# Performance work log

Hardware: AMD Instinct MI355X
Metric: run time of the kernel (lower is better)

The kernel has to match this reference:

```python
import jax, jax.numpy as jnp
import numpy as np

NUM_HEADS = 4
NUM_GROUPS = 8
EPS = 1e-5


def setup_inputs() -> dict:
    key = jax.random.key(0)
    ks = jax.random.split(key, 4)
    b, c, h, w = 16, 512, 32, 32
    x = jax.random.normal(ks[0], (b, c, h, w), dtype=jnp.float32)
    norm_gamma = jnp.ones((c,), dtype=jnp.float32)
    norm_beta = jnp.zeros((c,), dtype=jnp.float32)
    qkv_w = jax.random.normal(ks[1], (3 * c, c), dtype=jnp.float32) * (c ** -0.5)
    qkv_b = jnp.zeros((3 * c,), dtype=jnp.float32)
    proj_w = jax.random.normal(ks[2], (c, c), dtype=jnp.float32) * (c ** -0.5)
    proj_b = jnp.zeros((c,), dtype=jnp.float32)
    return {"x": x, "norm_gamma": norm_gamma, "norm_beta": norm_beta,
            "qkv_w": qkv_w, "qkv_b": qkv_b, "proj_w": proj_w, "proj_b": proj_b}


def reference(x, norm_gamma, norm_beta, qkv_w, qkv_b, proj_w, proj_b):
    b, c, h, w = x.shape
    nh = NUM_HEADS
    dh = c // nh
    n = h * w
    # GroupNorm(8, c): normalize over (c/G, h, w) within each group, biased var
    xg = x.reshape(b, NUM_GROUPS, -1)
    mu = jnp.mean(xg, axis=-1, keepdims=True)
    var = jnp.var(xg, axis=-1, keepdims=True)
    xn = ((xg - mu) * jax.lax.rsqrt(var + EPS)).reshape(b, c, h, w)
    xn = xn * norm_gamma[:, None, None] + norm_beta[:, None, None]
    # QKV 1x1 conv == channel matmul
    qkv = jnp.einsum('oc,bchw->bohw', qkv_w, xn) + qkv_b[:, None, None]
    q, k, v = jnp.split(qkv, 3, axis=1)  # each [b, c, h, w]

    def to_heads(t):  # [b, c, h, w] -> [b, nh, n, dh]
        return t.reshape(b, nh, dh, n).transpose(0, 1, 3, 2)

    q, k, v = to_heads(q), to_heads(k), to_heads(v)
    scale = dh ** -0.5
    attn = jax.nn.softmax(jnp.einsum('bhnd,bhmd->bhnm', q, k) * scale, axis=-1)
    out = jnp.einsum('bhnm,bhmd->bhnd', attn, v)  # [b, nh, n, dh]
    out = out.transpose(0, 1, 3, 2).reshape(b, c, h, w)
    out = jnp.einsum('oc,bchw->bohw', proj_w, out) + proj_b[:, None, None]
    return x + out
```

## Files before the change

### kernel.cpp

```cpp
#include <hip/hip_runtime.h>

typedef unsigned short u16;
typedef unsigned int   u32;

typedef __attribute__((ext_vector_type(8)))  short bf16x8;
typedef __attribute__((ext_vector_type(16))) float f32x16;
typedef __attribute__((ext_vector_type(2)))  unsigned int u32x2;
#define MFMA32(a, b, c) __builtin_amdgcn_mfma_f32_32x32x16_bf16(a, b, c, 0, 0, 0)

__device__ __forceinline__ float bf2f(u16 h) { return __uint_as_float(((u32)h) << 16); }
__device__ __forceinline__ u16 f2bf(float f) {
  u32 u = __float_as_uint(f);
  u += 0x7fffu + ((u >> 16) & 1u);
  return (u16)(u >> 16);
}
__device__ __forceinline__ void unpack8(uint4 u, float* f) {
  f[0] = __uint_as_float(u.x << 16); f[1] = __uint_as_float(u.x & 0xffff0000u);
  f[2] = __uint_as_float(u.y << 16); f[3] = __uint_as_float(u.y & 0xffff0000u);
  f[4] = __uint_as_float(u.z << 16); f[5] = __uint_as_float(u.z & 0xffff0000u);
  f[6] = __uint_as_float(u.w << 16); f[7] = __uint_as_float(u.w & 0xffff0000u);
}
__device__ __forceinline__ void unpack4(uint2 u, float* f) {
  f[0] = __uint_as_float(u.x << 16); f[1] = __uint_as_float(u.x & 0xffff0000u);
  f[2] = __uint_as_float(u.y << 16); f[3] = __uint_as_float(u.y & 0xffff0000u);
}

template <bool F>
__device__ __forceinline__ void load8(const void* p, size_t idx, float* f) {
  if constexpr (F) {
    const float4* q = (const float4*)((const float*)p + idx);
    float4 a = q[0], b = q[1];
    f[0] = a.x; f[1] = a.y; f[2] = a.z; f[3] = a.w;
    f[4] = b.x; f[5] = b.y; f[6] = b.z; f[7] = b.w;
  } else {
    unpack8(*(const uint4*)((const u16*)p + idx), f);
  }
}
template <bool F>
__device__ __forceinline__ void load4(const void* p, size_t idx, float* f) {
  if constexpr (F) {
    float4 a = *(const float4*)((const float*)p + idx);
    f[0] = a.x; f[1] = a.y; f[2] = a.z; f[3] = a.w;
  } else {
    unpack4(*(const uint2*)((const u16*)p + idx), f);
  }
}
template <bool F>
__device__ __forceinline__ float load1(const void* p, size_t idx) {
  if constexpr (F) return ((const float*)p)[idx];
  else return bf2f(((const u16*)p)[idx]);
}

__device__ __forceinline__ void gl2lds16(const void* g, void* l) {
  __builtin_amdgcn_global_load_lds(
      (const __attribute__((address_space(1))) void*)g,
      (__attribute__((address_space(3))) void*)l, 16, 0, 0);
}

__global__ void detect_dtype(const void* __restrict__ x, int* __restrict__ flag) {
  if (threadIdx.x == 0 && blockIdx.x == 0) {
    const u32* p = (const u32*)x;
    int sane = 0;
    for (int i = 0; i < 256; ++i) {
      u32 e = (p[i] >> 7) & 0xFFu;
      sane += (e >= 100u && e <= 150u) ? 1 : 0;
    }
    *flag = (sane < 192) ? 1 : 0;
  }
}

__global__ void signal_ws(u16* __restrict__ out, int n) {
  int i = blockIdx.x * 256 + threadIdx.x;
  if (i < n) out[i] = 0x42C8;
}

#define SM_SCALE 0.08838834764831843f
#define QSC 0.12751743f


__global__ void __launch_bounds__(256) wconv_rt(const void* __restrict__ qkvw,
                                                const void* __restrict__ qkvb,
                                                u16* __restrict__ dst,
                                                const int* __restrict__ flag) {
  const bool F = (flag[0] != 0);
  int i = (blockIdx.x * 256 + threadIdx.x) * 8;
  if (i >= 787968) return;
  if (!F) {
    uint4 v = (i < 786432) ? *(const uint4*)((const u16*)qkvw + i)
                           : *(const uint4*)((const u16*)qkvb + (i - 786432));
    *(uint4*)(dst + i) = v;
  } else {
    const float* src = (i < 786432) ? ((const float*)qkvw + i)
                                    : ((const float*)qkvb + (i - 786432));
    float f[8];
    float4 a = *(const float4*)src, b = *(const float4*)(src + 4);
    f[0]=a.x; f[1]=a.y; f[2]=a.z; f[3]=a.w; f[4]=b.x; f[5]=b.y; f[6]=b.z; f[7]=b.w;
    u32 w0 = (u32)f2bf(f[0]) | ((u32)f2bf(f[1]) << 16);
    u32 w1 = (u32)f2bf(f[2]) | ((u32)f2bf(f[3]) << 16);
    u32 w2 = (u32)f2bf(f[4]) | ((u32)f2bf(f[5]) << 16);
    u32 w3 = (u32)f2bf(f[6]) | ((u32)f2bf(f[7]) << 16);
    *(uint4*)(dst + i) = make_uint4(w0, w1, w2, w3);
  }
}

template <bool F>
__device__ __forceinline__ void gn_norm_body(
    const void* __restrict__ x, const void* __restrict__ gamma,
    const void* __restrict__ beta, u16* __restrict__ xT,
    int g, int b, int tid,
    float* ssum, float* ssq, float* scb, float* bsb, float (*Tf)[64][65]) {
  const size_t base = (size_t)(b * 512 + g * 64) * 1024;
  float sum = 0.f, sq = 0.f;
  for (int i = tid; i < 8192; i += 256) {
    float f[8]; load8<F>(x, base + (size_t)i * 8, f);
#pragma unroll
    for (int m = 0; m < 8; ++m) { sum += f[m]; sq += f[m] * f[m]; }
  }
  ssum[tid] = sum; ssq[tid] = sq; __syncthreads();
  for (int off = 128; off > 0; off >>= 1) {
    if (tid < off) { ssum[tid] += ssum[tid + off]; ssq[tid] += ssq[tid + off]; }
    __syncthreads();
  }
  if (tid < 64) {
    float mu  = ssum[0] * (1.f / 65536.f);
    float var = ssq[0] * (1.f / 65536.f) - mu * mu;
    float s = load1<F>(gamma, g * 64 + tid) * rsqrtf(var + 1e-5f);
    scb[tid] = s;
    bsb[tid] = load1<F>(beta, g * 64 + tid) - mu * s;
  }
  __syncthreads();

  for (int s0 = 0; s0 < 1024; s0 += 64) {
    const int pb = (s0 >> 6) & 1;
#pragma unroll
    for (int half = 0; half < 2; ++half) {
      int idx = tid + half * 256;
      int c_loc = idx >> 3, s8 = (idx & 7) * 8;
      float f[8];
      load8<F>(x, base + (size_t)c_loc * 1024 + s0 + s8, f);
      float sm = scb[c_loc], ba = bsb[c_loc];
#pragma unroll
      for (int m = 0; m < 8; ++m) Tf[pb][s8 + m][c_loc] = f[m] * sm + ba;
    }
    __syncthreads();
#pragma unroll
    for (int half = 0; half < 2; ++half) {
      int idx = tid + half * 256;
      int s_loc = idx >> 3, c8 = (idx & 7) * 8;
      u32 pk[4];
#pragma unroll
      for (int m = 0; m < 4; ++m)
        pk[m] = (u32)f2bf(Tf[pb][s_loc][c8 + 2 * m]) |
                ((u32)f2bf(Tf[pb][s_loc][c8 + 2 * m + 1]) << 16);
      *(uint4*)(xT + (size_t)(b * 1024 + s0 + s_loc) * 512 + g * 64 + c8) =
          make_uint4(pk[0], pk[1], pk[2], pk[3]);
    }
  }
}

__global__ void __launch_bounds__(256) gn_norm_rt(const void* __restrict__ x,
                                                  const void* __restrict__ gamma,
                                                  const void* __restrict__ beta,
                                                  u16* __restrict__ xT,
                                                  const int* __restrict__ flag) {
  __shared__ float ssum[256], ssq[256], scb[64], bsb[64];
  __shared__ float Tf[2][64][65];
  const int g = blockIdx.x, b = blockIdx.y, tid = threadIdx.x;
  if (flag[0] != 0) gn_norm_body<true >(x, gamma, beta, xT, g, b, tid, ssum, ssq, scb, bsb, Tf);
  else              gn_norm_body<false>(x, gamma, beta, xT, g, b, tid, ssum, ssq, scb, bsb, Tf);
}

__global__ void __launch_bounds__(256, 4)
gemm_qkv(const u16* __restrict__ xT, const u16* __restrict__ wbf,
         u16* __restrict__ qkT, u16* __restrict__ Vbuf) {
  const bool vrole = (blockIdx.y >= 8);
  const int n0 = blockIdx.x * 128;
  const int m0 = (vrole ? (int)blockIdx.y - 8 : (int)blockIdx.y) * 128;
  const int b  = blockIdx.z;
  __shared__ __align__(16) u16 At[8192];
  __shared__ __align__(16) u16 Bt[8192];
  const int tid = threadIdx.x;
  const int w = tid >> 6, lane = tid & 63;
  const int lo = lane & 31, hi = lane >> 5;
  const int wm = w >> 1, wn = w & 1;
  const u16* bias = wbf + 786432;
  const u16* Ab = vrole ? (wbf + 524288) : (xT + (size_t)b * 524288);
  const u16* Bb = vrole ? (xT + (size_t)b * 524288) : wbf;
  u16* outp = vrole ? (Vbuf + (size_t)b * 524288) : (qkT + (size_t)b * 1048576);
  const int srow = lane >> 3, spc = lane & 7;

  f32x16 cA[2][2];
#pragma unroll
  for (int i = 0; i < 2; ++i)
#pragma unroll
    for (int j = 0; j < 2; ++j)
#pragma unroll
      for (int r = 0; r < 16; ++r) cA[i][j][r] = 0.f;

  for (int kt = 0; kt < 8; ++kt) {
    const int kb = kt * 64;
#pragma unroll
    for (int c = 0; c < 4; ++c) {
      int grp = w * 4 + c;
      int row = grp * 8 + srow;
      int lc  = spc ^ (row & 7);
      gl2lds16(Ab + (size_t)(m0 + row) * 512 + kb + lc * 8, &At[grp * 512]);
      gl2lds16(Bb + (size_t)(n0 + row) * 512 + kb + lc * 8, &Bt[grp * 512]);
    }
    __syncthreads();
#pragma unroll
    for (int k16 = 0; k16 < 4; ++k16) {
      const int lc = k16 * 2 + hi;
      const int rA0 = wm * 64 + lo,  rA1 = rA0 + 32;
      const int rB0 = wn * 64 + lo,  rB1 = rB0 + 32;
      bf16x8 a0 = *(const bf16x8*)&At[rA0 * 64 + ((lc ^ (rA0 & 7)) << 3)];
      bf16x8 a1 = *(const bf16x8*)&At[rA1 * 64 + ((lc ^ (rA1 & 7)) << 3)];
      bf16x8 b0 = *(const bf16x8*)&Bt[rB0 * 64 + ((lc ^ (rB0 & 7)) << 3)];
      bf16x8 b1 = *(const bf16x8*)&Bt[rB1 * 64 + ((lc ^ (rB1 & 7)) << 3)];
      cA[0][0] = MFMA32(a0, b0, cA[0][0]);
      cA[0][1] = MFMA32(a0, b1, cA[0][1]);
      cA[1][0] = MFMA32(a1, b0, cA[1][0]);
      cA[1][1] = MFMA32(a1, b1, cA[1][1]);
    }
    __syncthreads();
  }

  float bcol[2] = {0.f, 0.f};
  if (!vrole) {
    bcol[0] = bf2f(bias[n0 + wn * 64 + lo]);
    bcol[1] = bf2f(bias[n0 + wn * 64 + 32 + lo]);
  }
#pragma unroll
  for (int mt = 0; mt < 2; ++mt)
#pragma unroll
    for (int nt = 0; nt < 2; ++nt) {
      const int nbase = n0 + wn * 64 + nt * 32;
#pragma unroll
      for (int r = 0; r < 16; ++r) {
        int m = m0 + wm * 64 + mt * 32 + (r & 3) + 8 * (r >> 2) + 4 * hi;
        int n = nbase + lo;
        float v = cA[mt][nt][r];
        if (!vrole) {
          v += bcol[nt];
          if (nbase < 512) v *= QSC;
        } else {
          v += bf2f(bias[1024 + m]);
        }
        outp[(size_t)m * 1024 + n] = f2bf(v);
      }
    }
}

template <bool F>
__device__ __forceinline__ void proj_body(const void* __restrict__ A,
                                          const u16* __restrict__ B,
                                          const void* __restrict__ bias,
                                          const void* __restrict__ resid,
                                          void* __restrict__ outp,
                                          int n0, int m0, int b, int tid,
                                          u16 (*At)[72], u16 (*Bt)[72]) {
  const int w = tid >> 6, lane = tid & 63;
  const int lo = lane & 31, hi = lane >> 5;
  const int wm = w >> 1, wn = w & 1;
  const size_t bBase = (size_t)b * 524288;

  f32x16 cA[2][2];
#pragma unroll
  for (int i = 0; i < 2; ++i)
#pragma unroll
    for (int j = 0; j < 2; ++j)
#pragma unroll
      for (int r = 0; r < 16; ++r) cA[i][j][r] = 0.f;

  for (int kt = 0; kt < 8; ++kt) {
#pragma unroll
    for (int i = 0; i < 4; ++i) {
      int idx = tid + i * 256;
      int row = idx >> 3, kc = (idx & 7) * 8;
      int k = kt * 64 + kc;
      {
        if constexpr (F) {
          float f[8]; load8<true>(A, (size_t)(m0 + row) * 512 + k, f);
          u32 w0 = (u32)f2bf(f[0]) | ((u32)f2bf(f[1]) << 16);
          u32 w1 = (u32)f2bf(f[2]) | ((u32)f2bf(f[3]) << 16);
          u32 w2 = (u32)f2bf(f[4]) | ((u32)f2bf(f[5]) << 16);
          u32 w3 = (u32)f2bf(f[6]) | ((u32)f2bf(f[7]) << 16);
          *(uint4*)&At[row][kc] = make_uint4(w0, w1, w2, w3);
        } else {
          *(uint4*)&At[row][kc] =
              *(const uint4*)((const u16*)A + (size_t)(m0 + row) * 512 + k);
        }
      }
      *(uint4*)&Bt[row][kc] =
          *(const uint4*)(B + bBase + (size_t)(n0 + row) * 512 + k);
    }
    __syncthreads();
#pragma unroll
    for (int k16 = 0; k16 < 4; ++k16) {
      const int ko = k16 * 16 + hi * 8;
      bf16x8 a0 = *(const bf16x8*)&At[wm * 64 + lo][ko];
      bf16x8 a1 = *(const bf16x8*)&At[wm * 64 + 32 + lo][ko];
      bf16x8 b0 = *(const bf16x8*)&Bt[wn * 64 + lo][ko];
      bf16x8 b1 = *(const bf16x8*)&Bt[wn * 64 + 32 + lo][ko];
      cA[0][0] = MFMA32(a0, b0, cA[0][0]);
      cA[0][1] = MFMA32(a0, b1, cA[0][1]);
      cA[1][0] = MFMA32(a1, b0, cA[1][0]);
      cA[1][1] = MFMA32(a1, b1, cA[1][1]);
    }
    __syncthreads();
  }

#pragma unroll
  for (int mt = 0; mt < 2; ++mt)
#pragma unroll
    for (int nt = 0; nt < 2; ++nt) {
#pragma unroll
      for (int r = 0; r < 16; ++r) {
        int m = m0 + wm * 64 + mt * 32 + (r & 3) + 8 * (r >> 2) + 4 * hi;
        int n = n0 + wn * 64 + nt * 32 + lo;
        float v = cA[mt][nt][r];
        v += load1<F>(bias, m);
        v += load1<F>(resid, bBase + (size_t)m * 1024 + n);
        size_t off = bBase + (size_t)m * 1024 + n;
        if constexpr (F) ((float*)outp)[off] = v;
        else             ((u16*)outp)[off] = f2bf(v);
      }
    }
}

__global__ void __launch_bounds__(256, 4)
proj_rt(const void* __restrict__ projw, const u16* __restrict__ aout,
        const void* __restrict__ projb, const void* __restrict__ x,
        void* __restrict__ outp, const int* __restrict__ flag) {
  __shared__ __align__(16) u16 At[128][72];
  __shared__ __align__(16) u16 Bt[128][72];
  const int n0 = blockIdx.x * 128, m0 = blockIdx.y * 128, b = blockIdx.z;
  if (flag[0] != 0) proj_body<true >(projw, aout, projb, x, outp, n0, m0, b, threadIdx.x, At, Bt);
  else              proj_body<false>(projw, aout, projb, x, outp, n0, m0, b, threadIdx.x, At, Bt);
}

__global__ void __launch_bounds__(256, 2) attn4(const u16* __restrict__ qkT,
                                                const u16* __restrict__ V,
                                                u16* __restrict__ aout) {
  const int bh = blockIdx.x;
  const int q0 = blockIdx.y * 128;
  const int b = bh >> 2, h = bh & 3;
  const u16* qt = qkT + (size_t)b * 1048576;
  const u16* vb = V + (size_t)b * 524288 + (size_t)(h * 128) * 1024;
  __shared__ __align__(16) u16 smem[32768];
  const int tid = threadIdx.x;
  const int w = tid >> 6, lane = tid & 63;
  const int lo = lane & 31, hi = lane >> 5;

#pragma unroll
  for (int c = 0; c < 8; ++c) {
    int grp = w * 8 + c;
    int row = grp * 4 + (lane >> 4);
    int lc  = (lane & 15) ^ (row & 7);
    gl2lds16(qt + (size_t)(q0 + row) * 1024 + h * 128 + lc * 8, &smem[grp * 512]);
  }
#pragma unroll
  for (int c = 0; c < 4; ++c) {
    int grp = w * 4 + c;
    { int row = grp * 4 + (lane >> 4);
      int lc  = (lane & 15) ^ (row & 7);
      gl2lds16(qt + (size_t)row * 1024 + 512 + h * 128 + lc * 8,
               &smem[16384 + grp * 512]); }
    { int row = grp * 8 + (lane >> 3);
      int lc  = (lane & 7) ^ (row & 7);
      gl2lds16(vb + (size_t)row * 1024 + lc * 8,
               &smem[16384 + 8192 + grp * 512]); }
  }
  __syncthreads();
  bf16x8 qf[8];
  {
    const int row = 32 * w + lo;
#pragma unroll
    for (int k16 = 0; k16 < 8; ++k16) {
      int lc = k16 * 2 + hi;
      qf[k16] = *(const bf16x8*)&smem[row * 128 + ((lc ^ (row & 7)) << 3)];
    }
  }
  __syncthreads();

  f32x16 o[4];
  float lp = 0.f;
#pragma unroll
  for (int dt = 0; dt < 4; ++dt)
#pragma unroll
    for (int r = 0; r < 16; ++r) o[dt][r] = 0.f;

  for (int kt = 0; kt < 16; ++kt) {
    const u16* rb = &smem[((kt & 1) ^ 1) << 14];
    u16* wbuf = &smem[(kt & 1) << 14];

    if (kt < 15) {
      const int k0n = (kt + 1) * 64;
#pragma unroll
      for (int c = 0; c < 4; ++c) {
        int grp = w * 4 + c;
        { int row = grp * 4 + (lane >> 4);
          int lc  = (lane & 15) ^ (row & 7);
          gl2lds16(qt + (size_t)(k0n + row) * 1024 + 512 + h * 128 + lc * 8,
                   wbuf + grp * 512); }
        { int row = grp * 8 + (lane >> 3);
          int lc  = (lane & 7) ^ (row & 7);
          gl2lds16(vb + (size_t)row * 1024 + k0n + lc * 8,
                   wbuf + 8192 + grp * 512); }
      }
    }

    f32x16 s0, s1;
#pragma unroll
    for (int r = 0; r < 16; ++r) { s0[r] = 0.f; s1[r] = 0.f; }
#pragma unroll
    for (int k16 = 0; k16 < 8; ++k16) {
      const int lc = k16 * 2 + hi;
      const int r0 = lo, r1 = lo + 32;
      bf16x8 kf0 = *(const bf16x8*)&rb[r0 * 128 + ((lc ^ (r0 & 7)) << 3)];
      bf16x8 kf1 = *(const bf16x8*)&rb[r1 * 128 + ((lc ^ (r1 & 7)) << 3)];
      s0 = MFMA32(kf0, qf[k16], s0);
      s1 = MFMA32(kf1, qf[k16], s1);
    }

#pragma unroll
    for (int r = 0; r < 16; ++r) {
      s0[r] = exp2f(s0[r]);
      s1[r] = exp2f(s1[r]);
      lp += s0[r] + s1[r];
    }

    bf16x8 pa[4];
#define MKPA(ps, rb0, dst) do {                                               \
      u32 qa0, qa1, qb0, qb1;                                                 \
      asm("v_cvt_pk_bf16_f32 %0, %1, %2" : "=v"(qa0)                          \
          : "v"((ps)[(rb0) + 0]), "v"((ps)[(rb0) + 1]));                      \
      asm("v_cvt_pk_bf16_f32 %0, %1, %2" : "=v"(qa1)                          \
          : "v"((ps)[(rb0) + 2]), "v"((ps)[(rb0) + 3]));                      \
      asm("v_cvt_pk_bf16_f32 %0, %1, %2" : "=v"(qb0)                          \
          : "v"((ps)[(rb0) + 4]), "v"((ps)[(rb0) + 5]));                      \
      asm("v_cvt_pk_bf16_f32 %0, %1, %2" : "=v"(qb1)                          \
          : "v"((ps)[(rb0) + 6]), "v"((ps)[(rb0) + 7]));                      \
      u32x2 r0 = __builtin_amdgcn_permlane32_swap(qa0, qb0, false, false);    \
      u32x2 r1 = __builtin_amdgcn_permlane32_swap(qa1, qb1, false, false);    \
      union { u32 u[4]; bf16x8 v8; } pk_;                                     \
      pk_.u[0] = r0[0]; pk_.u[1] = r1[0]; pk_.u[2] = r0[1]; pk_.u[3] = r1[1]; \
      dst = pk_.v8;                                                           \
    } while (0)
    MKPA(s0, 0, pa[0]);
    MKPA(s0, 8, pa[1]);
    MKPA(s1, 0, pa[2]);
    MKPA(s1, 8, pa[3]);
#undef MKPA

#pragma unroll
    for (int t = 0; t < 4; ++t) {
      const int lc = t * 2 + hi;
#pragma unroll
      for (int dt = 0; dt < 4; ++dt) {
        const int row = dt * 32 + lo;
        bf16x8 bv = *(const bf16x8*)&rb[8192 + row * 64 + ((lc ^ (row & 7)) << 3)];
        o[dt] = MFMA32(pa[t], bv, o[dt]);
      }
    }
    __syncthreads();
  }

  float linv = 1.f / (lp + __shfl_xor(lp, 32));
#pragma unroll
  for (int r = 0; r < 16; ++r) {
    int pat = (r & 3) + 8 * (r >> 2) + 4 * hi;
    float lr = __shfl(linv, pat);
    int q = q0 + 32 * w + pat;
    size_t base = (size_t)(b * 1024 + q) * 512 + h * 128;
    aout[base +  0 + lo] = f2bf(o[0][r] * lr);
    aout[base + 32 + lo] = f2bf(o[1][r] * lr);
    aout[base + 64 + lo] = f2bf(o[2][r] * lr);
    aout[base + 96 + lo] = f2bf(o[3][r] * lr);
  }
}


template <bool F>
__global__ void __launch_bounds__(256) gn_stats(const void* __restrict__ x,
                                                const void* __restrict__ gamma,
                                                const void* __restrict__ beta,
                                                float* __restrict__ sc,
                                                float* __restrict__ bs,
                                                const int* __restrict__ flag) {
  if ((flag[0] != 0) != F) return;
  const int g = blockIdx.x, b = blockIdx.y;
  const int tid = threadIdx.x;
  const size_t base = (size_t)(b * 512 + g * 64) * 1024;
  float sum = 0.f, sq = 0.f;
  for (int i = tid; i < 8192; i += 256) {
    float f[8]; load8<F>(x, base + (size_t)i * 8, f);
#pragma unroll
    for (int m = 0; m < 8; ++m) { sum += f[m]; sq += f[m] * f[m]; }
  }
  __shared__ float ssum[256], ssq[256];
  ssum[tid] = sum; ssq[tid] = sq; __syncthreads();
  for (int off = 128; off > 0; off >>= 1) {
    if (tid < off) { ssum[tid] += ssum[tid + off]; ssq[tid] += ssq[tid + off]; }
    __syncthreads();
  }
  if (tid < 64) {
    float mu  = ssum[0] * (1.f / 65536.f);
    float var = ssq[0] * (1.f / 65536.f) - mu * mu;
    int c = g * 64 + tid;
    float s = load1<F>(gamma, c) * rsqrtf(var + 1e-5f);
    sc[b * 512 + c] = s;
    bs[b * 512 + c] = load1<F>(beta, c) - mu * s;
  }
}

template <bool F, bool BEXT, bool FOUT>
__global__ void __launch_bounds__(256) gemm64(const void* __restrict__ A,
                                              const void* __restrict__ B,
                                              const float* __restrict__ sc,
                                              const float* __restrict__ bs,
                                              const void* __restrict__ bias,
                                              const void* __restrict__ resid,
                                              void* __restrict__ outp,
                                              int mrows, int donorm, int bstride,
                                              const int* __restrict__ flag) {
  if ((flag[0] != 0) != F) return;
  const int s0 = blockIdx.x * 64;
  const int o0 = blockIdx.y * 64;
  const int b  = blockIdx.z;
  __shared__ __align__(16) float At[64][36];
  __shared__ __align__(16) float Bt[64][36];
  const int tid = threadIdx.x;
  const int ty = tid >> 4, tx = tid & 15;
  const int i0 = ty * 4, j0 = tx * 4;
  const int arow = tid >> 2, akc = (tid & 3) * 8;
  const int brow = tid >> 3, bnc = (tid & 7) * 8;
  float acc[4][4] = {};

  for (int kt = 0; kt < 512; kt += 32) {
    float af[8];
    load8<F>(A, (size_t)(o0 + arow) * 512 + akc + kt, af);
    *(float4*)&At[arow][akc]     = make_float4(af[0], af[1], af[2], af[3]);
    *(float4*)&At[arow][akc + 4] = make_float4(af[4], af[5], af[6], af[7]);
    const int c = kt + brow;
    float bf[8];
    load8<(BEXT && F)>(B, (size_t)(b * bstride + c) * 1024 + s0 + bnc, bf);
    float smul = 1.f, badd = 0.f;
    if (donorm) { smul = sc[b * 512 + c]; badd = bs[b * 512 + c]; }
#pragma unroll
    for (int m = 0; m < 8; ++m) Bt[bnc + m][brow] = bf[m] * smul + badd;
    __syncthreads();
#pragma unroll
    for (int kq = 0; kq < 8; ++kq) {
      float4 a0 = *(const float4*)&At[i0 + 0][kq * 4];
      float4 a1 = *(const float4*)&At[i0 + 1][kq * 4];
      float4 a2 = *(const float4*)&At[i0 + 2][kq * 4];
      float4 a3 = *(const float4*)&At[i0 + 3][kq * 4];
      float4 c0 = *(const float4*)&Bt[j0 + 0][kq * 4];
      float4 c1 = *(const float4*)&Bt[j0 + 1][kq * 4];
      float4 c2 = *(const float4*)&Bt[j0 + 2][kq * 4];
      float4 c3 = *(const float4*)&Bt[j0 + 3][kq * 4];
#define DOT4(ii, jj, AV, CV) acc[ii][jj] += AV.x * CV.x + AV.y * CV.y + AV.z * CV.z + AV.w * CV.w;
      DOT4(0,0,a0,c0) DOT4(0,1,a0,c1) DOT4(0,2,a0,c2) DOT4(0,3,a0,c3)
      DOT4(1,0,a1,c0) DOT4(1,1,a1,c1) DOT4(1,2,a1,c2) DOT4(1,3,a1,c3)
      DOT4(2,0,a2,c0) DOT4(2,1,a2,c1) DOT4(2,2,a2,c2) DOT4(2,3,a2,c3)
      DOT4(3,0,a3,c0) DOT4(3,1,a3,c1) DOT4(3,2,a3,c2) DOT4(3,3,a3,c3)
#undef DOT4
    }
    __syncthreads();
  }
#pragma unroll
  for (int ii = 0; ii < 4; ++ii) {
    const int o = o0 + i0 + ii;
    const float bb = load1<F>(bias, o);
    float v[4];
#pragma unroll
    for (int jj = 0; jj < 4; ++jj) v[jj] = acc[ii][jj] + bb;
    if (resid) {
      float xf[4];
      load4<F>(resid, (size_t)(b * 512 + o) * 1024 + s0 + j0, xf);
#pragma unroll
      for (int jj = 0; jj < 4; ++jj) v[jj] += xf[jj];
    }
    const size_t ooff = (size_t)(b * mrows + o) * 1024 + s0 + j0;
    if constexpr (FOUT) {
      *(float4*)((float*)outp + ooff) = make_float4(v[0], v[1], v[2], v[3]);
    } else {
      uint2 pk;
      pk.x = (u32)f2bf(v[0]) | ((u32)f2bf(v[1]) << 16);
      pk.y = (u32)f2bf(v[2]) | ((u32)f2bf(v[3]) << 16);
      *(uint2*)((u16*)outp + ooff) = pk;
    }
  }
}

__global__ void __launch_bounds__(256, 2) attn_old(u16* __restrict__ qkv) {
  const int q0 = blockIdx.x * 128;
  const int bh = blockIdx.y;
  const int b = bh >> 2, h = bh & 3;
  u16* qp = qkv + (size_t)(b * 1536 + h * 128) * 1024;
  const u16* kp = qp + (size_t)512 * 1024;
  const u16* vp = qp + (size_t)1024 * 1024;
  __shared__ __align__(16) u16 Qt[128][136];
  __shared__ __align__(16) u16 Kt[32][136];
  __shared__ __align__(16) u16 Vt[128][40];
  __shared__ __align__(16) u16 Pt[128][40];
  const int tid = threadIdx.x;
  const int w = tid >> 6, lane = tid & 63;
  const int lo = lane & 31, hi = lane >> 5;

  for (int idx = tid; idx < 2048; idx += 256) {
    int d = idx >> 4, s8 = (idx & 15) * 8;
    uint4 qv = *(const uint4*)(qp + (size_t)d * 1024 + q0 + s8);
    const u16* qs = (const u16*)&qv;
#pragma unroll
    for (int m = 0; m < 8; ++m) Qt[s8 + m][d] = qs[m];
  }
  __syncthreads();
  bf16x8 qf[8];
#pragma unroll
  for (int kq = 0; kq < 8; ++kq)
    qf[kq] = *(const bf16x8*)&Qt[32 * w + lo][kq * 16 + hi * 8];

  f32x16 o0, o1, o2, o3;
  float lp[16];
#pragma unroll
  for (int r = 0; r < 16; ++r) { o0[r] = 0.f; o1[r] = 0.f; o2[r] = 0.f; o3[r] = 0.f; lp[r] = 0.f; }

  for (int kt = 0; kt < 32; ++kt) {
    const int k0 = kt * 32;
    __syncthreads();
    for (int idx = tid; idx < 512; idx += 256) {
      int d = idx >> 2, s8 = (idx & 3) * 8;
      uint4 kv = *(const uint4*)(kp + (size_t)d * 1024 + k0 + s8);
      const u16* ks = (const u16*)&kv;
#pragma unroll
      for (int m = 0; m < 8; ++m) Kt[s8 + m][d] = ks[m];
      *(uint4*)&Vt[d][s8] = *(const uint4*)(vp + (size_t)d * 1024 + k0 + s8);
    }
    __syncthreads();
    f32x16 acc;
#pragma unroll
    for (int r = 0; r < 16; ++r) acc[r] = 0.f;
#pragma unroll
    for (int kq = 0; kq < 8; ++kq) {
      bf16x8 bq = *(const bf16x8*)&Kt[lo][kq * 16 + hi * 8];
      acc = MFMA32(qf[kq], bq, acc);
    }
#pragma unroll
    for (int r = 0; r < 16; ++r) {
      float pe = __expf(acc[r] * SM_SCALE);
      lp[r] += pe;
      int row = (r & 3) + 8 * (r >> 2) + 4 * hi;
      Pt[32 * w + row][lo] = f2bf(pe);
    }
    __syncthreads();
#pragma unroll
    for (int kq2 = 0; kq2 < 2; ++kq2) {
      bf16x8 a2 = *(const bf16x8*)&Pt[32 * w + lo][kq2 * 16 + hi * 8];
      bf16x8 b0 = *(const bf16x8*)&Vt[ 0 + lo][kq2 * 16 + hi * 8];
      bf16x8 b1 = *(const bf16x8*)&Vt[32 + lo][kq2 * 16 + hi * 8];
      bf16x8 b2 = *(const bf16x8*)&Vt[64 + lo][kq2 * 16 + hi * 8];
      bf16x8 b3 = *(const bf16x8*)&Vt[96 + lo][kq2 * 16 + hi * 8];
      o0 = MFMA32(a2, b0, o0);
      o1 = MFMA32(a2, b1, o1);
      o2 = MFMA32(a2, b2, o2);
      o3 = MFMA32(a2, b3, o3);
    }
  }
#pragma unroll
  for (int r = 0; r < 16; ++r) {
    float su = lp[r];
    su += __shfl_xor(su, 1);  su += __shfl_xor(su, 2);
    su += __shfl_xor(su, 4);  su += __shfl_xor(su, 8);
    su += __shfl_xor(su, 16);
    float linv = 1.f / su;
    int row = (r & 3) + 8 * (r >> 2) + 4 * hi;
    int q = q0 + 32 * w + row;
    size_t base = (size_t)(b * 1536 + h * 128) * 1024 + q;
    qkv[base + (size_t)( 0 + lo) * 1024] = f2bf(o0[r] * linv);
    qkv[base + (size_t)(32 + lo) * 1024] = f2bf(o1[r] * linv);
    qkv[base + (size_t)(64 + lo) * 1024] = f2bf(o2[r] * linv);
    qkv[base + (size_t)(96 + lo) * 1024] = f2bf(o3[r] * linv);
  }
}

extern "C" void kernel_launch(void* const* d_in, const int* in_sizes, int n_in,
                              void* d_out, int out_size, void* d_ws, size_t ws_size,
                              hipStream_t stream) {
  const void* x     = d_in[0];
  const void* gamma = d_in[1];
  const void* beta  = d_in[2];
  const void* qkvw  = d_in[3];
  const void* qkvb  = d_in[4];
  const void* projw = d_in[5];
  const void* projb = d_in[6];

  char* ws = (char*)d_ws;
  const size_t MB = 1024 * 1024;
  const size_t FAST_NEED = 64 * MB + 64;
  const size_t OLD_NEED  = 48 * MB + 256 + 2 * 16 * 512 * 4;

  if (ws_size >= FAST_NEED) {
    u16* xT   = (u16*)ws;
    u16* qkT  = (u16*)(ws + 16 * MB);
    u16* Vbuf = (u16*)(ws + 48 * MB);
    int* flag = (int*)(ws + 64 * MB);
    u16* wbf  = (u16*)d_out;

    detect_dtype<<<1, 64, 0, stream>>>(x, flag);
    wconv_rt<<<385, 256, 0, stream>>>(qkvw, qkvb, wbf, flag);
    gn_norm_rt<<<dim3(8, 16), 256, 0, stream>>>(x, gamma, beta, xT, flag);

    gemm_qkv<<<dim3(8, 12, 16), 256, 0, stream>>>(xT, wbf, qkT, Vbuf);

    attn4<<<dim3(64, 8), 256, 0, stream>>>(qkT, Vbuf, xT);

    proj_rt<<<dim3(8, 4, 16), 256, 0, stream>>>(projw, xT, projb, x, d_out, flag);
    return;
  }

  if (ws_size < OLD_NEED) {
    signal_ws<<<(out_size + 255) / 256, 256, 0, stream>>>((u16*)d_out, out_size);
    return;
  }

  const size_t QKV_BYTES = (size_t)16 * 1536 * 1024 * 2;
  u16* qkv  = (u16*)ws;
  int* flag = (int*)(ws + QKV_BYTES);
  float* sc = (float*)(ws + QKV_BYTES + 256);
  float* bs = sc + 16 * 512;

  detect_dtype<<<1, 64, 0, stream>>>(x, flag);
  gn_stats<false><<<dim3(8, 16), 256, 0, stream>>>(x, gamma, beta, sc, bs, flag);
  gn_stats<true ><<<dim3(8, 16), 256, 0, stream>>>(x, gamma, beta, sc, bs, flag);
  gemm64<false, true, false><<<dim3(16, 24, 16), 256, 0, stream>>>(
      qkvw, x, sc, bs, qkvb, nullptr, qkv, 1536, 1, 512, flag);
  gemm64<true, true, false><<<dim3(16, 24, 16), 256, 0, stream>>>(
      qkvw, x, sc, bs, qkvb, nullptr, qkv, 1536, 1, 512, flag);
  attn_old<<<dim3(8, 64), 256, 0, stream>>>(qkv);
  gemm64<false, false, false><<<dim3(16, 8, 16), 256, 0, stream>>>(
      projw, qkv, sc, bs, projb, x, d_out, 512, 0, 1536, flag);
  gemm64<true, false, true><<<dim3(16, 8, 16), 256, 0, stream>>>(
      projw, qkv, sc, bs, projb, x, d_out, 512, 0, 1536, flag);
}
```

Measured before the change: 262.6 us.

## Split GroupNorm into parallel stats pass and spatial-chunk apply pass

Replaces the single GroupNorm kernel (128 blocks, each reducing and then normalizing one group) with two kernels. The first computes partial sums over half-groups across 256 blocks, and the second normalizes and transposes one 64-position spatial chunk per block across all channels, also 256 blocks. The goal is better GPU occupancy for this memory-bound stage. In exchange, x is read twice across the two launches, and an extra launch plus a small partials buffer are placed inside d_out.

```diff
diff --git a/kernel.cpp b/kernel.cpp
--- a/kernel.cpp
+++ b/kernel.cpp
@@ -104,14 +104,13 @@
 }
 
 template <bool F>
-__device__ __forceinline__ void gn_norm_body(
-    const void* __restrict__ x, const void* __restrict__ gamma,
-    const void* __restrict__ beta, u16* __restrict__ xT,
-    int g, int b, int tid,
-    float* ssum, float* ssq, float* scb, float* bsb, float (*Tf)[64][65]) {
-  const size_t base = (size_t)(b * 512 + g * 64) * 1024;
+__device__ __forceinline__ void gn_stats2_body(const void* __restrict__ x,
+                                               float* __restrict__ part,
+                                               int g, int b, int half, int tid,
+                                               float* ssum, float* ssq) {
+  const size_t base = (size_t)(b * 512 + g * 64 + half * 32) * 1024;
   float sum = 0.f, sq = 0.f;
-  for (int i = tid; i < 8192; i += 256) {
+  for (int i = tid; i < 4096; i += 256) {
     float f[8]; load8<F>(x, base + (size_t)i * 8, f);
 #pragma unroll
     for (int m = 0; m < 8; ++m) { sum += f[m]; sq += f[m] * f[m]; }
@@ -121,24 +120,50 @@
     if (tid < off) { ssum[tid] += ssum[tid + off]; ssq[tid] += ssq[tid + off]; }
     __syncthreads();
   }
-  if (tid < 64) {
-    float mu  = ssum[0] * (1.f / 65536.f);
-    float var = ssq[0] * (1.f / 65536.f) - mu * mu;
-    float s = load1<F>(gamma, g * 64 + tid) * rsqrtf(var + 1e-5f);
-    scb[tid] = s;
-    bsb[tid] = load1<F>(beta, g * 64 + tid) - mu * s;
+  if (tid == 0) {
+    part[(b * 8 + g) * 4 + half * 2 + 0] = ssum[0];
+    part[(b * 8 + g) * 4 + half * 2 + 1] = ssq[0];
+  }
+}
+
+__global__ void __launch_bounds__(256) gn_stats2(const void* __restrict__ x,
+                                                 float* __restrict__ part,
+                                                 const int* __restrict__ flag) {
+  __shared__ float ssum[256], ssq[256];
+  const int g = blockIdx.x, b = blockIdx.y, half = blockIdx.z, tid = threadIdx.x;
+  if (flag[0] != 0) gn_stats2_body<true >(x, part, g, b, half, tid, ssum, ssq);
+  else              gn_stats2_body<false>(x, part, g, b, half, tid, ssum, ssq);
+}
+
+template <bool F>
+__device__ __forceinline__ void gn_apply_body(
+    const void* __restrict__ x, const void* __restrict__ gamma,
+    const void* __restrict__ beta, const float* __restrict__ part,
+    u16* __restrict__ xT, int chunk, int b, int tid,
+    float* scb, float* bsb, float (*Tf)[64][65]) {
+  const int s0 = chunk * 64;
+  for (int c = tid; c < 512; c += 256) {
+    int gg = c >> 6;
+    const float* p = part + (b * 8 + gg) * 4;
+    float sum = p[0] + p[2], sq = p[1] + p[3];
+    float mu  = sum * (1.f / 65536.f);
+    float var = sq * (1.f / 65536.f) - mu * mu;
+    float s = load1<F>(gamma, c) * rsqrtf(var + 1e-5f);
+    scb[c] = s;
+    bsb[c] = load1<F>(beta, c) - mu * s;
   }
   __syncthreads();
 
-  for (int s0 = 0; s0 < 1024; s0 += 64) {
-    const int pb = (s0 >> 6) & 1;
+  for (int gb = 0; gb < 8; ++gb) {
+    const int pb = gb & 1;
 #pragma unroll
     for (int half = 0; half < 2; ++half) {
       int idx = tid + half * 256;
       int c_loc = idx >> 3, s8 = (idx & 7) * 8;
+      int c = gb * 64 + c_loc;
       float f[8];
-      load8<F>(x, base + (size_t)c_loc * 1024 + s0 + s8, f);
-      float sm = scb[c_loc], ba = bsb[c_loc];
+      load8<F>(x, (size_t)(b * 512 + c) * 1024 + s0 + s8, f);
+      float sm = scb[c], ba = bsb[c];
 #pragma unroll
       for (int m = 0; m < 8; ++m) Tf[pb][s8 + m][c_loc] = f[m] * sm + ba;
     }
@@ -152,22 +177,23 @@
       for (int m = 0; m < 4; ++m)
         pk[m] = (u32)f2bf(Tf[pb][s_loc][c8 + 2 * m]) |
                 ((u32)f2bf(Tf[pb][s_loc][c8 + 2 * m + 1]) << 16);
-      *(uint4*)(xT + (size_t)(b * 1024 + s0 + s_loc) * 512 + g * 64 + c8) =
+      *(uint4*)(xT + (size_t)(b * 1024 + s0 + s_loc) * 512 + gb * 64 + c8) =
           make_uint4(pk[0], pk[1], pk[2], pk[3]);
     }
   }
 }
 
-__global__ void __launch_bounds__(256) gn_norm_rt(const void* __restrict__ x,
-                                                  const void* __restrict__ gamma,
-                                                  const void* __restrict__ beta,
-                                                  u16* __restrict__ xT,
-                                                  const int* __restrict__ flag) {
-  __shared__ float ssum[256], ssq[256], scb[64], bsb[64];
+__global__ void __launch_bounds__(256) gn_apply(const void* __restrict__ x,
+                                                const void* __restrict__ gamma,
+                                                const void* __restrict__ beta,
+                                                const float* __restrict__ part,
+                                                u16* __restrict__ xT,
+                                                const int* __restrict__ flag) {
+  __shared__ float scb[512], bsb[512];
   __shared__ float Tf[2][64][65];
-  const int g = blockIdx.x, b = blockIdx.y, tid = threadIdx.x;
-  if (flag[0] != 0) gn_norm_body<true >(x, gamma, beta, xT, g, b, tid, ssum, ssq, scb, bsb, Tf);
-  else              gn_norm_body<false>(x, gamma, beta, xT, g, b, tid, ssum, ssq, scb, bsb, Tf);
+  const int chunk = blockIdx.x, b = blockIdx.y, tid = threadIdx.x;
+  if (flag[0] != 0) gn_apply_body<true >(x, gamma, beta, part, xT, chunk, b, tid, scb, bsb, Tf);
+  else              gn_apply_body<false>(x, gamma, beta, part, xT, chunk, b, tid, scb, bsb, Tf);
 }
 
 __global__ void __launch_bounds__(256, 4)
@@ -707,10 +733,12 @@
     u16* Vbuf = (u16*)(ws + 48 * MB);
     int* flag = (int*)(ws + 64 * MB);
     u16* wbf  = (u16*)d_out;
+    float* part = (float*)((char*)d_out + 2 * MB);
 
     detect_dtype<<<1, 64, 0, stream>>>(x, flag);
     wconv_rt<<<385, 256, 0, stream>>>(qkvw, qkvb, wbf, flag);
-    gn_norm_rt<<<dim3(8, 16), 256, 0, stream>>>(x, gamma, beta, xT, flag);
+    gn_stats2<<<dim3(8, 16, 2), 256, 0, stream>>>(x, part, flag);
+    gn_apply<<<dim3(16, 16), 256, 0, stream>>>(x, gamma, beta, part, xT, flag);
 
     gemm_qkv<<<dim3(8, 12, 16), 256, 0, stream>>>(xT, wbf, qkT, Vbuf);
 
```

New measurement: 237.7 us. -9.5%, faster.
